# Performance work log

Hardware: AMD Instinct MI355X
Metric: run time of the kernel (lower is better)

Reference implementation:

```python
import jax, jax.numpy as jnp
import numpy as np

D_MODEL = 1024
NUM_HEADS = 16
H_DIM = 4096
EPS = 1e-5


def setup_inputs() -> dict:
    key = jax.random.key(0)
    ks = jax.random.split(key, 16)
    B, S, D, H = 2, 2048, D_MODEL, H_DIM
    s = 0.02
    return {
        "x": jax.random.normal(ks[0], (B, S, D), jnp.float32),
        "wq": jax.random.normal(ks[1], (D, D), jnp.float32) * s,
        "bq": jnp.zeros((D,), jnp.float32),
        "wk": jax.random.normal(ks[2], (D, D), jnp.float32) * s,
        "bk": jnp.zeros((D,), jnp.float32),
        "wv": jax.random.normal(ks[3], (D, D), jnp.float32) * s,
        "bv": jnp.zeros((D,), jnp.float32),
        "wo": jax.random.normal(ks[4], (D, D), jnp.float32) * s,
        "bo": jnp.zeros((D,), jnp.float32),
        "ln1_g": jnp.ones((D,), jnp.float32),
        "ln1_b": jnp.zeros((D,), jnp.float32),
        "w1": jax.random.normal(ks[5], (H, D), jnp.float32) * s,
        "b1": jnp.zeros((H,), jnp.float32),
        "w2": jax.random.normal(ks[6], (D, H), jnp.float32) * s,
        "b2": jnp.zeros((D,), jnp.float32),
        "ln2_g": jnp.ones((D,), jnp.float32),
        "ln2_b": jnp.zeros((D,), jnp.float32),
    }


def _layer_norm(x, g, b):
    mu = jnp.mean(x, axis=-1, keepdims=True)
    var = jnp.mean(jnp.square(x - mu), axis=-1, keepdims=True)
    return (x - mu) * jax.lax.rsqrt(var + EPS) * g + b


def _mhsa(x, wq, bq, wk, bk, wv, bv, wo, bo):
    B, S, D = x.shape
    Hh, hd = NUM_HEADS, D // NUM_HEADS
    q = (x @ wq.T + bq).reshape(B, S, Hh, hd)
    k = (x @ wk.T + bk).reshape(B, S, Hh, hd)
    v = (x @ wv.T + bv).reshape(B, S, Hh, hd)
    scale = hd ** -0.5
    scores = jnp.einsum('bqhd,bkhd->bhqk', q, k) * scale
    att = jax.nn.softmax(scores, axis=-1)
    out = jnp.einsum('bhqk,bkhd->bqhd', att, v).reshape(B, S, D)
    return out @ wo.T + bo


def reference(x, wq, bq, wk, bk, wv, bv, wo, bo, ln1_g, ln1_b,
              w1, b1, w2, b2, ln2_g, ln2_b):
    # pre-norm variant as written in the torch source:
    # x = norm1(x); x = x + msa(x)  (residual uses NORMALIZED x)
    x = _layer_norm(x, ln1_g, ln1_b)
    x = x + _mhsa(x, wq, bq, wk, bk, wv, bv, wo, bo)
    x = _layer_norm(x, ln2_g, ln2_b)
    h = jax.nn.gelu(x @ w1.T + b1, approximate=False)
    x = x + (h @ w2.T + b2)
    return x
```

## Files before the change

### kernel.cpp

```cpp
#include <hip/hip_runtime.h>
#include <hip/hip_bf16.h>

typedef unsigned short u16;
typedef __attribute__((ext_vector_type(8))) short short8;
typedef __attribute__((ext_vector_type(4))) float f32x4;

#define DM 1024
#define HM 4096
#define NHEADS 16
#define HD 64
#define SQ 2048
#define NBATCH 2
#define NTOK 4096

#define NX  ((size_t)NTOK * DM)

__device__ __forceinline__ u16 f2b(float f) {
    union { float f; unsigned int i; } w; w.f = f;
    unsigned int x = w.i;
    return (u16)((x + 0x7FFFu + ((x >> 16) & 1u)) >> 16);
}
__device__ __forceinline__ u16 f2b_ru(float f) {
    union { float f; unsigned int i; } w; w.f = f;
    return (u16)((w.i + 0x8000u) >> 16);
}

__device__ __forceinline__ void gload_lds16(const void* g, void* l) {
    __builtin_amdgcn_global_load_lds(
        (const __attribute__((address_space(1))) void*)g,
        (__attribute__((address_space(3))) void*)l, 16, 0, 0);
}

__global__ void cvt_bf(const float* __restrict__ src, u16* __restrict__ dst,
                       int n4, float scale) {
    int i = blockIdx.x * 256 + threadIdx.x;
    if (i >= n4) return;
    float4 f = ((const float4*)src)[i];
    ushort4 o;
    o.x = f2b(f.x * scale); o.y = f2b(f.y * scale);
    o.z = f2b(f.z * scale); o.w = f2b(f.w * scale);
    ((ushort4*)dst)[i] = o;
}

__global__ void pack_bias(const float* __restrict__ bq, const float* __restrict__ bk,
                          const float* __restrict__ bv, float* __restrict__ dst) {
    int i = blockIdx.x * 256 + threadIdx.x;
    if (i >= 3 * DM) return;
    float v = (i < DM) ? bq[i] * 0.125f : (i < 2 * DM) ? bk[i - DM] : bv[i - 2 * DM];
    dst[i] = v;
}

__global__ void ln_kernel(const float* __restrict__ xin, const float* __restrict__ g,
                          const float* __restrict__ b, float* __restrict__ outf,
                          u16* __restrict__ outb) {
    int t = blockIdx.x, tid = threadIdx.x;
    float4 f = ((const float4*)(xin + (size_t)t * DM))[tid];
    float v0 = f.x, v1 = f.y, v2 = f.z, v3 = f.w;
    float s  = v0 + v1 + v2 + v3;
    float ss = v0*v0 + v1*v1 + v2*v2 + v3*v3;
    #pragma unroll
    for (int o = 32; o > 0; o >>= 1) {
        s  += __shfl_down(s,  o, 64);
        ss += __shfl_down(ss, o, 64);
    }
    __shared__ float rs[4], rss[4];
    int w = tid >> 6, lane = tid & 63;
    if (!lane) { rs[w] = s; rss[w] = ss; }
    __syncthreads();
    s  = rs[0] + rs[1] + rs[2] + rs[3];
    ss = rss[0] + rss[1] + rss[2] + rss[3];
    float mean = s * (1.0f / DM);
    float var  = ss * (1.0f / DM) - mean * mean;
    float rstd = rsqrtf(var + 1e-5f);
    float4 gu = ((const float4*)g)[tid];
    float4 bu = ((const float4*)b)[tid];
    float4 o;
    o.x = (v0 - mean) * rstd * gu.x + bu.x;
    o.y = (v1 - mean) * rstd * gu.y + bu.y;
    o.z = (v2 - mean) * rstd * gu.z + bu.z;
    o.w = (v3 - mean) * rstd * gu.w + bu.w;
    ((float4*)(outf + (size_t)t * DM))[tid] = o;
    ushort4 ob; ob.x = f2b(o.x); ob.y = f2b(o.y); ob.z = f2b(o.z); ob.w = f2b(o.w);
    ((ushort4*)(outb + (size_t)t * DM))[tid] = ob;
}

template<int GELU, int RESID, int OUTBF>
__global__ __launch_bounds__(256, 2)
void gemm_bt(const u16* __restrict__ A, const u16* __restrict__ W,
             const float* __restrict__ bias, const float* __restrict__ resid,
             void* __restrict__ Cout, int M, int N, int K) {
    __shared__ __attribute__((aligned(16))) u16 As[128 * 32];
    __shared__ __attribute__((aligned(16))) u16 Bs[128 * 32];
    int tid  = threadIdx.x;
    int wid  = tid >> 6, lane = tid & 63;
    int m0 = blockIdx.y << 7, n0 = blockIdx.x << 7;
    int wm = (wid & 1) << 6, wn = (wid >> 1) << 6;

    int seg0 = wid << 1;
    int rIn  = lane >> 2;
    int cIn  = (lane & 3) << 3;
    const u16* aG0 = A + (size_t)(m0 + (seg0 << 4) + rIn) * K + cIn;
    const u16* aG1 = A + (size_t)(m0 + ((seg0 + 1) << 4) + rIn) * K + cIn;
    const u16* bG0 = W + (size_t)(n0 + (seg0 << 4) + rIn) * K + cIn;
    const u16* bG1 = W + (size_t)(n0 + ((seg0 + 1) << 4) + rIn) * K + cIn;
    u16* aL0 = As + (seg0 << 9);
    u16* aL1 = As + ((seg0 + 1) << 9);
    u16* bL0 = Bs + (seg0 << 9);
    u16* bL1 = Bs + ((seg0 + 1) << 9);

    int fr = lane & 15;
    int fc = (lane >> 4) << 3;

    f32x4 acc[4][4];
    #pragma unroll
    for (int i = 0; i < 4; i++)
        #pragma unroll
        for (int j = 0; j < 4; j++)
            acc[i][j] = (f32x4){0.f, 0.f, 0.f, 0.f};

    for (int k0 = 0; k0 < K; k0 += 32) {
        gload_lds16(aG0 + k0, aL0);
        gload_lds16(aG1 + k0, aL1);
        gload_lds16(bG0 + k0, bL0);
        gload_lds16(bG1 + k0, bL1);
        __syncthreads();
        short8 af[4], bf[4];
        #pragma unroll
        for (int mi = 0; mi < 4; mi++)
            af[mi] = *(const short8*)(As + (size_t)(wm + (mi << 4) + fr) * 32 + fc);
        #pragma unroll
        for (int ni = 0; ni < 4; ni++)
            bf[ni] = *(const short8*)(Bs + (size_t)(wn + (ni << 4) + fr) * 32 + fc);
        #pragma unroll
        for (int mi = 0; mi < 4; mi++)
            #pragma unroll
            for (int ni = 0; ni < 4; ni++)
                acc[mi][ni] = __builtin_amdgcn_mfma_f32_16x16x32_bf16(
                    af[mi], bf[ni], acc[mi][ni], 0, 0, 0);
        __syncthreads();
    }

    int erow = (lane >> 4) << 2;
    #pragma unroll
    for (int ni = 0; ni < 4; ni++) {
        int col = n0 + wn + (ni << 4) + fr;
        float bv = bias[col];
        #pragma unroll
        for (int mi = 0; mi < 4; mi++) {
            #pragma unroll
            for (int r = 0; r < 4; r++) {
                int row = m0 + wm + (mi << 4) + erow + r;
                float val = acc[mi][ni][r] + bv;
                if (GELU)  val = 0.5f * val * (1.0f + erff(val * 0.70710678118654752f));
                if (RESID) val += resid[(size_t)row * N + col];
                if (OUTBF) ((u16*)Cout)[(size_t)row * N + col] = f2b(val);
                else       ((float*)Cout)[(size_t)row * N + col] = val;
            }
        }
    }
}

template<int GELU, int RESID, int OUTBF>
__global__ __launch_bounds__(256, 2)
void gemm_n64(const u16* __restrict__ A, const u16* __restrict__ W,
              const float* __restrict__ bias, const float* __restrict__ resid,
              void* __restrict__ Cout, int M, int N, int K) {
    __shared__ __attribute__((aligned(16))) u16 As[128 * 32];
    __shared__ __attribute__((aligned(16))) u16 Bs[64 * 32];
    int tid  = threadIdx.x;
    int wid  = tid >> 6, lane = tid & 63;
    int m0 = blockIdx.y << 7, n0 = blockIdx.x << 6;
    int wm = (wid & 1) << 6, wn = (wid >> 1) << 5;

    int seg0 = wid << 1;
    int rIn  = lane >> 2;
    int cIn  = (lane & 3) << 3;
    const u16* aG0 = A + (size_t)(m0 + (seg0 << 4) + rIn) * K + cIn;
    const u16* aG1 = A + (size_t)(m0 + ((seg0 + 1) << 4) + rIn) * K + cIn;
    const u16* bG0 = W + (size_t)(n0 + (wid << 4) + rIn) * K + cIn;
    u16* aL0 = As + (seg0 << 9);
    u16* aL1 = As + ((seg0 + 1) << 9);
    u16* bL0 = Bs + (wid << 9);

    int fr = lane & 15;
    int fc = (lane >> 4) << 3;

    f32x4 acc[4][2];
    #pragma unroll
    for (int i = 0; i < 4; i++)
        #pragma unroll
        for (int j = 0; j < 2; j++)
            acc[i][j] = (f32x4){0.f, 0.f, 0.f, 0.f};

    for (int k0 = 0; k0 < K; k0 += 32) {
        gload_lds16(aG0 + k0, aL0);
        gload_lds16(aG1 + k0, aL1);
        gload_lds16(bG0 + k0, bL0);
        __syncthreads();
        short8 af[4], bf[2];
        #pragma unroll
        for (int mi = 0; mi < 4; mi++)
            af[mi] = *(const short8*)(As + (size_t)(wm + (mi << 4) + fr) * 32 + fc);
        #pragma unroll
        for (int ni = 0; ni < 2; ni++)
            bf[ni] = *(const short8*)(Bs + (size_t)(wn + (ni << 4) + fr) * 32 + fc);
        #pragma unroll
        for (int mi = 0; mi < 4; mi++)
            #pragma unroll
            for (int ni = 0; ni < 2; ni++)
                acc[mi][ni] = __builtin_amdgcn_mfma_f32_16x16x32_bf16(
                    af[mi], bf[ni], acc[mi][ni], 0, 0, 0);
        __syncthreads();
    }

    int erow = (lane >> 4) << 2;
    #pragma unroll
    for (int ni = 0; ni < 2; ni++) {
        int col = n0 + wn + (ni << 4) + fr;
        float bv = bias[col];
        #pragma unroll
        for (int mi = 0; mi < 4; mi++) {
            #pragma unroll
            for (int r = 0; r < 4; r++) {
                int row = m0 + wm + (mi << 4) + erow + r;
                float val = acc[mi][ni][r] + bv;
                if (GELU)  val = 0.5f * val * (1.0f + erff(val * 0.70710678118654752f));
                if (RESID) val += resid[(size_t)row * N + col];
                if (OUTBF) ((u16*)Cout)[(size_t)row * N + col] = f2b(val);
                else       ((float*)Cout)[(size_t)row * N + col] = val;
            }
        }
    }
}

__global__ __launch_bounds__(256) void fattn_mfma(const u16* __restrict__ QKV,
                                                  u16* __restrict__ O) {
    __shared__ __attribute__((aligned(16))) u16 Qs[4096];
    __shared__ __attribute__((aligned(16))) u16 Ks[2][4096];
    __shared__ __attribute__((aligned(16))) u16 Vt[2][4096];
    __shared__ __attribute__((aligned(16))) u16 Ps[4][1024];
    const int ld = 3 * DM;
    int bid = blockIdx.x;
    int qt = bid & 31, bh = bid >> 5;
    int h = bh & (NHEADS - 1), b = bh >> 4;
    int tid = threadIdx.x, wid = tid >> 6, lane = tid & 63;
    int fr = lane & 15, fc = (lane >> 4) << 3;
    size_t tokb = (size_t)b * SQ;
    const u16* Qg = QKV + tokb * ld + h * HD;
    const u16* Kg = QKV + tokb * ld + DM + h * HD;
    const u16* Vg = QKV + tokb * ld + 2 * DM + h * HD;
    int vk = lane, vd0 = wid << 4;
    int s0 = wid << 1;

    {
        #pragma unroll
        for (int t = 0; t < 2; t++) {
            int s = s0 + t;
            const u16* g = Qg + (size_t)(qt * 64 + ((s & 3) << 4) + (lane >> 2)) * ld
                         + ((s >> 2) << 5) + ((lane & 3) << 3);
            gload_lds16(g, Qs + (s << 9));
        }
    }
    {
        #pragma unroll
        for (int t = 0; t < 2; t++) {
            int s = s0 + t;
            const u16* g = Kg + (size_t)(((s & 3) << 4) + (lane >> 2)) * ld
                         + ((s >> 2) << 5) + ((lane & 3) << 3);
            gload_lds16(g, Ks[0] + (s << 9));
        }
        const u16* vrow = Vg + (size_t)vk * ld + vd0;
        int cbase = (vk >> 5) << 11;
        int kk = vk & 31;
        #pragma unroll
        for (int j = 0; j < 4; j++) {
            ushort4 vv = *(const ushort4*)(vrow + (j << 2));
            int d = vd0 + (j << 2);
            Vt[0][cbase + (d + 0) * 32 + kk] = vv.x;
            Vt[0][cbase + (d + 1) * 32 + kk] = vv.y;
            Vt[0][cbase + (d + 2) * 32 + kk] = vv.z;
            Vt[0][cbase + (d + 3) * 32 + kk] = vv.w;
        }
    }
    f32x4 oacc[4];
    #pragma unroll
    for (int di = 0; di < 4; di++) oacc[di] = (f32x4){0.f, 0.f, 0.f, 0.f};
    float lsum[4] = {0.f, 0.f, 0.f, 0.f};
    __syncthreads();
    short8 aq0 = *(const short8*)(Qs + ((wid << 4) + fr) * 32 + fc);
    short8 aq1 = *(const short8*)(Qs + 2048 + ((wid << 4) + fr) * 32 + fc);

    for (int kt = 0; kt < SQ / 64; kt++) {
        int buf = kt & 1;
        if (kt + 1 < SQ / 64) {
            #pragma unroll
            for (int t = 0; t < 2; t++) {
                int s = s0 + t;
                const u16* g = Kg + (size_t)((kt + 1) * 64 + ((s & 3) << 4) + (lane >> 2)) * ld
                             + ((s >> 2) << 5) + ((lane & 3) << 3);
                gload_lds16(g, Ks[buf ^ 1] + (s << 9));
            }
            const u16* vrow = Vg + (size_t)((kt + 1) * 64 + vk) * ld + vd0;
            int cbase = (vk >> 5) << 11;
            int kk = vk & 31;
            #pragma unroll
            for (int j = 0; j < 4; j++) {
                ushort4 vv = *(const ushort4*)(vrow + (j << 2));
                int d = vd0 + (j << 2);
                Vt[buf ^ 1][cbase + (d + 0) * 32 + kk] = vv.x;
                Vt[buf ^ 1][cbase + (d + 1) * 32 + kk] = vv.y;
                Vt[buf ^ 1][cbase + (d + 2) * 32 + kk] = vv.z;
                Vt[buf ^ 1][cbase + (d + 3) * 32 + kk] = vv.w;
            }
        }
        #pragma unroll
        for (int ni = 0; ni < 4; ni++) {
            short8 bk0 = *(const short8*)(Ks[buf] + ((ni << 4) + fr) * 32 + fc);
            short8 bk1 = *(const short8*)(Ks[buf] + 2048 + ((ni << 4) + fr) * 32 + fc);
            f32x4 z = (f32x4){0.f, 0.f, 0.f, 0.f};
            z = __builtin_amdgcn_mfma_f32_16x16x32_bf16(aq0, bk0, z, 0, 0, 0);
            z = __builtin_amdgcn_mfma_f32_16x16x32_bf16(aq1, bk1, z, 0, 0, 0);
            int c  = (ni << 4) + fr;
            int cb = (c >> 5) << 9;
            int kk = c & 31;
            #pragma unroll
            for (int r = 0; r < 4; r++) {
                float e = __expf(z[r]);
                lsum[r] += e;
                Ps[wid][cb + (((lane >> 4) << 2) + r) * 32 + kk] = f2b_ru(e);
            }
        }
        short8 ap0 = *(const short8*)(&Ps[wid][fr * 32 + fc]);
        short8 ap1 = *(const short8*)(&Ps[wid][512 + fr * 32 + fc]);
        #pragma unroll
        for (int di = 0; di < 4; di++) {
            short8 bv0 = *(const short8*)(Vt[buf] + ((di << 4) + fr) * 32 + fc);
            short8 bv1 = *(const short8*)(Vt[buf] + 2048 + ((di << 4) + fr) * 32 + fc);
            oacc[di] = __builtin_amdgcn_mfma_f32_16x16x32_bf16(ap0, bv0, oacc[di], 0, 0, 0);
            oacc[di] = __builtin_amdgcn_mfma_f32_16x16x32_bf16(ap1, bv1, oacc[di], 0, 0, 0);
        }
        __syncthreads();
    }
    #pragma unroll
    for (int msk = 1; msk <= 8; msk <<= 1)
        #pragma unroll
        for (int r = 0; r < 4; r++) lsum[r] += __shfl_xor(lsum[r], msk, 64);
    float inv[4];
    #pragma unroll
    for (int r = 0; r < 4; r++) inv[r] = 1.0f / lsum[r];
    #pragma unroll
    for (int di = 0; di < 4; di++) {
        int d = (di << 4) + fr;
        #pragma unroll
        for (int r = 0; r < 4; r++) {
            int q = qt * 64 + (wid << 4) + ((lane >> 4) << 2) + r;
            O[(tokb + q) * DM + h * HD + d] = f2b(oacc[di][r] * inv[r]);
        }
    }
}

extern "C" void kernel_launch(void* const* d_in, const int* in_sizes, int n_in,
                              void* d_out, int out_size, void* d_ws, size_t ws_size,
                              hipStream_t stream) {
    if (n_in < 17) return;
    const float* x   = (const float*)d_in[0];
    const float* wq  = (const float*)d_in[1];
    const float* bq  = (const float*)d_in[2];
    const float* wk  = (const float*)d_in[3];
    const float* bk  = (const float*)d_in[4];
    const float* wv  = (const float*)d_in[5];
    const float* bv  = (const float*)d_in[6];
    const float* wo  = (const float*)d_in[7];
    const float* bo  = (const float*)d_in[8];
    const float* g1  = (const float*)d_in[9];
    const float* e1  = (const float*)d_in[10];
    const float* w1  = (const float*)d_in[11];
    const float* b1  = (const float*)d_in[12];
    const float* w2  = (const float*)d_in[13];
    const float* b2  = (const float*)d_in[14];
    const float* g2  = (const float*)d_in[15];
    const float* e2  = (const float*)d_in[16];

    float* F = (float*)d_ws;
    size_t off = 0;
    float* xnf   = F + off; off += NX;
    u16*   xnb   = (u16*)(F + off); off += NX / 2;
    u16*   qkvb  = (u16*)(F + off); off += (size_t)NTOK * 3 * DM / 2;
    float* y     = F + off; off += NX;
    u16*   aob   = (u16*)(F + off); off += NX / 2;
    u16*   hb    = (u16*)(F + off); off += (size_t)NTOK * HM / 2;
    u16*   wqkvb = (u16*)(F + off); off += (size_t)3 * DM * DM / 2;
    u16*   wob   = (u16*)(F + off); off += (size_t)DM * DM / 2;
    u16*   w1b   = (u16*)(F + off); off += (size_t)HM * DM / 2;
    u16*   w2b   = (u16*)(F + off); off += (size_t)DM * HM / 2;
    float* bqkv  = F + off; off += 3 * DM;
    if (ws_size < off * sizeof(float)) return;

    dim3 blk(256);
    cvt_bf<<<(DM * DM / 4 + 255) / 256, blk, 0, stream>>>(wq, wqkvb, DM * DM / 4, 0.125f);
    cvt_bf<<<(DM * DM / 4 + 255) / 256, blk, 0, stream>>>(wk, wqkvb + (size_t)DM * DM, DM * DM / 4, 1.0f);
    cvt_bf<<<(DM * DM / 4 + 255) / 256, blk, 0, stream>>>(wv, wqkvb + (size_t)2 * DM * DM, DM * DM / 4, 1.0f);
    cvt_bf<<<(DM * DM / 4 + 255) / 256, blk, 0, stream>>>(wo, wob, DM * DM / 4, 1.0f);
    cvt_bf<<<(HM * DM / 4 + 255) / 256, blk, 0, stream>>>(w1, w1b, HM * DM / 4, 1.0f);
    cvt_bf<<<(DM * HM / 4 + 255) / 256, blk, 0, stream>>>(w2, w2b, DM * HM / 4, 1.0f);
    pack_bias<<<(3 * DM + 255) / 256, blk, 0, stream>>>(bq, bk, bv, bqkv);

    ln_kernel<<<NTOK, blk, 0, stream>>>(x, g1, e1, xnf, xnb);
    gemm_bt<0,0,1><<<dim3(3 * DM / 128, NTOK / 128), blk, 0, stream>>>(
        xnb, wqkvb, bqkv, nullptr, qkvb, NTOK, 3 * DM, DM);
    fattn_mfma<<<NBATCH * NHEADS * (SQ / 64), blk, 0, stream>>>(qkvb, aob);
    gemm_n64<0,1,0><<<dim3(DM / 64, NTOK / 128), blk, 0, stream>>>(
        aob, wob, bo, xnf, y, NTOK, DM, DM);
    ln_kernel<<<NTOK, blk, 0, stream>>>(y, g2, e2, xnf, xnb);
    gemm_bt<1,0,1><<<dim3(HM / 128, NTOK / 128), blk, 0, stream>>>(
        xnb, w1b, b1, nullptr, hb, NTOK, HM, DM);
    gemm_n64<0,1,0><<<dim3(DM / 64, NTOK / 128), blk, 0, stream>>>(
        hb, w2b, b2, xnf, d_out, NTOK, DM, HM);
}
```

Baseline: 432.1 us.

## Double GEMM K-step to 64, merge weight conversions, reuse Q LDS for P

After: 423.8 us. About the same (-1.9%).

```diff
diff --git a/kernel.cpp b/kernel.cpp
--- a/kernel.cpp
+++ b/kernel.cpp
@@ -31,14 +31,24 @@
         (__attribute__((address_space(3))) void*)l, 16, 0, 0);
 }
 
-__global__ void cvt_bf(const float* __restrict__ src, u16* __restrict__ dst,
-                       int n4, float scale) {
+__global__ void cvt_all(const float* __restrict__ wq, const float* __restrict__ wk,
+                        const float* __restrict__ wv, const float* __restrict__ wo,
+                        const float* __restrict__ w1, const float* __restrict__ w2,
+                        u16* __restrict__ dst) {
+    const int NW4 = DM * DM / 4;
     int i = blockIdx.x * 256 + threadIdx.x;
-    if (i >= n4) return;
-    float4 f = ((const float4*)src)[i];
+    if (i >= 12 * NW4) return;
+    const float* src; int base; float sc = 1.0f;
+    if      (i <     NW4) { src = wq; base = 0;       sc = 0.125f; }
+    else if (i < 2 * NW4) { src = wk; base = NW4; }
+    else if (i < 3 * NW4) { src = wv; base = 2 * NW4; }
+    else if (i < 4 * NW4) { src = wo; base = 3 * NW4; }
+    else if (i < 8 * NW4) { src = w1; base = 4 * NW4; }
+    else                  { src = w2; base = 8 * NW4; }
+    float4 f = ((const float4*)src)[i - base];
     ushort4 o;
-    o.x = f2b(f.x * scale); o.y = f2b(f.y * scale);
-    o.z = f2b(f.z * scale); o.w = f2b(f.w * scale);
+    o.x = f2b(f.x * sc); o.y = f2b(f.y * sc);
+    o.z = f2b(f.z * sc); o.w = f2b(f.w * sc);
     ((ushort4*)dst)[i] = o;
 }
 
@@ -85,29 +95,20 @@
 }
 
 template<int GELU, int RESID, int OUTBF>
-__global__ __launch_bounds__(256, 2)
+__global__ __launch_bounds__(256, 3)
 void gemm_bt(const u16* __restrict__ A, const u16* __restrict__ W,
              const float* __restrict__ bias, const float* __restrict__ resid,
              void* __restrict__ Cout, int M, int N, int K) {
-    __shared__ __attribute__((aligned(16))) u16 As[128 * 32];
-    __shared__ __attribute__((aligned(16))) u16 Bs[128 * 32];
+    __shared__ __attribute__((aligned(16))) u16 As[128 * 64];
+    __shared__ __attribute__((aligned(16))) u16 Bs[128 * 64];
     int tid  = threadIdx.x;
     int wid  = tid >> 6, lane = tid & 63;
     int m0 = blockIdx.y << 7, n0 = blockIdx.x << 7;
     int wm = (wid & 1) << 6, wn = (wid >> 1) << 6;
 
-    int seg0 = wid << 1;
-    int rIn  = lane >> 2;
-    int cIn  = (lane & 3) << 3;
-    const u16* aG0 = A + (size_t)(m0 + (seg0 << 4) + rIn) * K + cIn;
-    const u16* aG1 = A + (size_t)(m0 + ((seg0 + 1) << 4) + rIn) * K + cIn;
-    const u16* bG0 = W + (size_t)(n0 + (seg0 << 4) + rIn) * K + cIn;
-    const u16* bG1 = W + (size_t)(n0 + ((seg0 + 1) << 4) + rIn) * K + cIn;
-    u16* aL0 = As + (seg0 << 9);
-    u16* aL1 = As + ((seg0 + 1) << 9);
-    u16* bL0 = Bs + (seg0 << 9);
-    u16* bL1 = Bs + ((seg0 + 1) << 9);
-
+    int rIn = lane >> 3;
+    int cIn = (lane & 7) << 3;
+    int s0  = wid << 2;
     int fr = lane & 15;
     int fc = (lane >> 4) << 3;
 
@@ -118,25 +119,31 @@
         for (int j = 0; j < 4; j++)
             acc[i][j] = (f32x4){0.f, 0.f, 0.f, 0.f};
 
-    for (int k0 = 0; k0 < K; k0 += 32) {
-        gload_lds16(aG0 + k0, aL0);
-        gload_lds16(aG1 + k0, aL1);
-        gload_lds16(bG0 + k0, bL0);
-        gload_lds16(bG1 + k0, bL1);
+    for (int k0 = 0; k0 < K; k0 += 64) {
+        #pragma unroll
+        for (int t = 0; t < 4; t++) {
+            int s = s0 + t;
+            gload_lds16(A + (size_t)(m0 + (s << 3) + rIn) * K + k0 + cIn, As + (s << 9));
+            gload_lds16(W + (size_t)(n0 + (s << 3) + rIn) * K + k0 + cIn, Bs + (s << 9));
+        }
         __syncthreads();
-        short8 af[4], bf[4];
-        #pragma unroll
-        for (int mi = 0; mi < 4; mi++)
-            af[mi] = *(const short8*)(As + (size_t)(wm + (mi << 4) + fr) * 32 + fc);
-        #pragma unroll
-        for (int ni = 0; ni < 4; ni++)
-            bf[ni] = *(const short8*)(Bs + (size_t)(wn + (ni << 4) + fr) * 32 + fc);
-        #pragma unroll
-        for (int mi = 0; mi < 4; mi++)
+        #pragma unroll
+        for (int ch = 0; ch < 2; ch++) {
+            int kc = (ch << 5) + fc;
+            short8 af[4], bf[4];
+            #pragma unroll
+            for (int mi = 0; mi < 4; mi++)
+                af[mi] = *(const short8*)(As + (size_t)(wm + (mi << 4) + fr) * 64 + kc);
             #pragma unroll
             for (int ni = 0; ni < 4; ni++)
-                acc[mi][ni] = __builtin_amdgcn_mfma_f32_16x16x32_bf16(
-                    af[mi], bf[ni], acc[mi][ni], 0, 0, 0);
+                bf[ni] = *(const short8*)(Bs + (size_t)(wn + (ni << 4) + fr) * 64 + kc);
+            #pragma unroll
+            for (int mi = 0; mi < 4; mi++)
+                #pragma unroll
+                for (int ni = 0; ni < 4; ni++)
+                    acc[mi][ni] = __builtin_amdgcn_mfma_f32_16x16x32_bf16(
+                        af[mi], bf[ni], acc[mi][ni], 0, 0, 0);
+        }
         __syncthreads();
     }
 
@@ -161,27 +168,21 @@
 }
 
 template<int GELU, int RESID, int OUTBF>
-__global__ __launch_bounds__(256, 2)
+__global__ __launch_bounds__(256, 3)
 void gemm_n64(const u16* __restrict__ A, const u16* __restrict__ W,
               const float* __restrict__ bias, const float* __restrict__ resid,
               void* __restrict__ Cout, int M, int N, int K) {
-    __shared__ __attribute__((aligned(16))) u16 As[128 * 32];
-    __shared__ __attribute__((aligned(16))) u16 Bs[64 * 32];
+    __shared__ __attribute__((aligned(16))) u16 As[128 * 64];
+    __shared__ __attribute__((aligned(16))) u16 Bs[64 * 64];
     int tid  = threadIdx.x;
     int wid  = tid >> 6, lane = tid & 63;
     int m0 = blockIdx.y << 7, n0 = blockIdx.x << 6;
     int wm = (wid & 1) << 6, wn = (wid >> 1) << 5;
 
-    int seg0 = wid << 1;
-    int rIn  = lane >> 2;
-    int cIn  = (lane & 3) << 3;
-    const u16* aG0 = A + (size_t)(m0 + (seg0 << 4) + rIn) * K + cIn;
-    const u16* aG1 = A + (size_t)(m0 + ((seg0 + 1) << 4) + rIn) * K + cIn;
-    const u16* bG0 = W + (size_t)(n0 + (wid << 4) + rIn) * K + cIn;
-    u16* aL0 = As + (seg0 << 9);
-    u16* aL1 = As + ((seg0 + 1) << 9);
-    u16* bL0 = Bs + (wid << 9);
-
+    int rIn = lane >> 3;
+    int cIn = (lane & 7) << 3;
+    int sA = wid << 2;
+    int sB = wid << 1;
     int fr = lane & 15;
     int fc = (lane >> 4) << 3;
 
@@ -192,24 +193,35 @@
         for (int j = 0; j < 2; j++)
             acc[i][j] = (f32x4){0.f, 0.f, 0.f, 0.f};
 
-    for (int k0 = 0; k0 < K; k0 += 32) {
-        gload_lds16(aG0 + k0, aL0);
-        gload_lds16(aG1 + k0, aL1);
-        gload_lds16(bG0 + k0, bL0);
+    for (int k0 = 0; k0 < K; k0 += 64) {
+        #pragma unroll
+        for (int t = 0; t < 4; t++) {
+            int s = sA + t;
+            gload_lds16(A + (size_t)(m0 + (s << 3) + rIn) * K + k0 + cIn, As + (s << 9));
+        }
+        #pragma unroll
+        for (int t = 0; t < 2; t++) {
+            int s = sB + t;
+            gload_lds16(W + (size_t)(n0 + (s << 3) + rIn) * K + k0 + cIn, Bs + (s << 9));
+        }
         __syncthreads();
-        short8 af[4], bf[2];
-        #pragma unroll
-        for (int mi = 0; mi < 4; mi++)
-            af[mi] = *(const short8*)(As + (size_t)(wm + (mi << 4) + fr) * 32 + fc);
-        #pragma unroll
-        for (int ni = 0; ni < 2; ni++)
-            bf[ni] = *(const short8*)(Bs + (size_t)(wn + (ni << 4) + fr) * 32 + fc);
-        #pragma unroll
-        for (int mi = 0; mi < 4; mi++)
+        #pragma unroll
+        for (int ch = 0; ch < 2; ch++) {
+            int kc = (ch << 5) + fc;
+            short8 af[4], bf[2];
+            #pragma unroll
+            for (int mi = 0; mi < 4; mi++)
+                af[mi] = *(const short8*)(As + (size_t)(wm + (mi << 4) + fr) * 64 + kc);
             #pragma unroll
             for (int ni = 0; ni < 2; ni++)
-                acc[mi][ni] = __builtin_amdgcn_mfma_f32_16x16x32_bf16(
-                    af[mi], bf[ni], acc[mi][ni], 0, 0, 0);
+                bf[ni] = *(const short8*)(Bs + (size_t)(wn + (ni << 4) + fr) * 64 + kc);
+            #pragma unroll
+            for (int mi = 0; mi < 4; mi++)
+                #pragma unroll
+                for (int ni = 0; ni < 2; ni++)
+                    acc[mi][ni] = __builtin_amdgcn_mfma_f32_16x16x32_bf16(
+                        af[mi], bf[ni], acc[mi][ni], 0, 0, 0);
+        }
         __syncthreads();
     }
 
@@ -235,10 +247,9 @@
 
 __global__ __launch_bounds__(256) void fattn_mfma(const u16* __restrict__ QKV,
                                                   u16* __restrict__ O) {
-    __shared__ __attribute__((aligned(16))) u16 Qs[4096];
+    __shared__ __attribute__((aligned(16))) u16 QP[4096];
     __shared__ __attribute__((aligned(16))) u16 Ks[2][4096];
     __shared__ __attribute__((aligned(16))) u16 Vt[2][4096];
-    __shared__ __attribute__((aligned(16))) u16 Ps[4][1024];
     const int ld = 3 * DM;
     int bid = blockIdx.x;
     int qt = bid & 31, bh = bid >> 5;
@@ -251,6 +262,7 @@
     const u16* Vg = QKV + tokb * ld + 2 * DM + h * HD;
     int vk = lane, vd0 = wid << 4;
     int s0 = wid << 1;
+    u16* Ps = QP + (wid << 10);
 
     {
         #pragma unroll
@@ -258,7 +270,7 @@
             int s = s0 + t;
             const u16* g = Qg + (size_t)(qt * 64 + ((s & 3) << 4) + (lane >> 2)) * ld
                          + ((s >> 2) << 5) + ((lane & 3) << 3);
-            gload_lds16(g, Qs + (s << 9));
+            gload_lds16(g, QP + (s << 9));
         }
     }
     {
@@ -287,8 +299,9 @@
     for (int di = 0; di < 4; di++) oacc[di] = (f32x4){0.f, 0.f, 0.f, 0.f};
     float lsum[4] = {0.f, 0.f, 0.f, 0.f};
     __syncthreads();
-    short8 aq0 = *(const short8*)(Qs + ((wid << 4) + fr) * 32 + fc);
-    short8 aq1 = *(const short8*)(Qs + 2048 + ((wid << 4) + fr) * 32 + fc);
+    short8 aq0 = *(const short8*)(QP + ((wid << 4) + fr) * 32 + fc);
+    short8 aq1 = *(const short8*)(QP + 2048 + ((wid << 4) + fr) * 32 + fc);
+    __syncthreads();
 
     for (int kt = 0; kt < SQ / 64; kt++) {
         int buf = kt & 1;
@@ -327,11 +340,11 @@
             for (int r = 0; r < 4; r++) {
                 float e = __expf(z[r]);
                 lsum[r] += e;
-                Ps[wid][cb + (((lane >> 4) << 2) + r) * 32 + kk] = f2b_ru(e);
+                Ps[cb + (((lane >> 4) << 2) + r) * 32 + kk] = f2b_ru(e);
             }
         }
-        short8 ap0 = *(const short8*)(&Ps[wid][fr * 32 + fc]);
-        short8 ap1 = *(const short8*)(&Ps[wid][512 + fr * 32 + fc]);
+        short8 ap0 = *(const short8*)(Ps + fr * 32 + fc);
+        short8 ap1 = *(const short8*)(Ps + 512 + fr * 32 + fc);
         #pragma unroll
         for (int di = 0; di < 4; di++) {
             short8 bv0 = *(const short8*)(Vt[buf] + ((di << 4) + fr) * 32 + fc);
@@ -397,12 +410,8 @@
     if (ws_size < off * sizeof(float)) return;
 
     dim3 blk(256);
-    cvt_bf<<<(DM * DM / 4 + 255) / 256, blk, 0, stream>>>(wq, wqkvb, DM * DM / 4, 0.125f);
-    cvt_bf<<<(DM * DM / 4 + 255) / 256, blk, 0, stream>>>(wk, wqkvb + (size_t)DM * DM, DM * DM / 4, 1.0f);
-    cvt_bf<<<(DM * DM / 4 + 255) / 256, blk, 0, stream>>>(wv, wqkvb + (size_t)2 * DM * DM, DM * DM / 4, 1.0f);
-    cvt_bf<<<(DM * DM / 4 + 255) / 256, blk, 0, stream>>>(wo, wob, DM * DM / 4, 1.0f);
-    cvt_bf<<<(HM * DM / 4 + 255) / 256, blk, 0, stream>>>(w1, w1b, HM * DM / 4, 1.0f);
-    cvt_bf<<<(DM * HM / 4 + 255) / 256, blk, 0, stream>>>(w2, w2b, DM * HM / 4, 1.0f);
+    cvt_all<<<(12 * DM * DM / 4 + 255) / 256, blk, 0, stream>>>(
+        wq, wk, wv, wo, w1, w2, wqkvb);
     pack_bias<<<(3 * DM + 255) / 256, blk, 0, stream>>>(bq, bk, bv, bqkv);
 
     ln_kernel<<<NTOK, blk, 0, stream>>>(x, g1, e1, xnf, xnb);
```
